# Optimization experiments

Hardware: AMD Instinct MI355X
Metric: run time of the kernel (lower is better)

## Reference

```python
import jax, jax.numpy as jnp
import numpy as np

EPS = 1e-5  # torch BatchNorm1d default eps


def setup_inputs() -> dict:
    key = jax.random.key(0)
    ks = jax.random.split(key, 8)
    B, H, D, DO = 8192, 8, 512, 256
    return {
        "x_concepts_encoded": jax.random.normal(ks[0], (B, H, D), dtype=jnp.float32),
        "relevance_weights": jax.random.uniform(ks[1], (B, H), dtype=jnp.float32),
        "bn_gamma": jax.random.uniform(ks[2], (D,), dtype=jnp.float32) + 0.5,
        "bn_beta": jax.random.normal(ks[3], (D,), dtype=jnp.float32) * 0.1,
        "bn_mean": jax.random.normal(ks[4], (D,), dtype=jnp.float32) * 0.1,
        "bn_var": jax.random.uniform(ks[5], (D,), dtype=jnp.float32) + 0.5,
        "W": jax.random.normal(ks[6], (DO, D), dtype=jnp.float32) / np.sqrt(D),
        "b": jax.random.normal(ks[7], (DO,), dtype=jnp.float32) * 0.01,
    }


def reference(x_concepts_encoded, relevance_weights, bn_gamma, bn_beta, bn_mean, bn_var, W, b):
    B, H = relevance_weights.shape
    x = x_concepts_encoded.reshape(B * H, -1)            # [B*H, D]
    # BatchNorm1d (inference: running stats) fused as scale/shift
    inv = bn_gamma * jax.lax.rsqrt(bn_var + EPS)
    h = x * inv + (bn_beta - bn_mean * inv)              # [B*H, D]
    # Swish
    h = h * jax.nn.sigmoid(h)
    # Linear
    out = h @ W.T + b                                    # [B*H, DO]
    # relevance-weighted sum over heads
    out = jnp.einsum('bhd,bh->bd', out.reshape(B, H, -1), relevance_weights)
    return out
```

## Files before the change

### kernel.cpp

```cpp
#include <hip/hip_runtime.h>
#include <hip/hip_bf16.h>

#define NB 8192
#define NH 8
#define ND 512
#define NO 256
#define ROWS 16

typedef __attribute__((ext_vector_type(8))) short short8;
typedef __attribute__((ext_vector_type(4))) float f32x4;

__device__ __align__(16) ushort g_wb[NO * ND];

__device__ __forceinline__ ushort f2bf(float f) {
    union { float f; unsigned u; } v; v.f = f;
    unsigned u = v.u;
    unsigned r = u + 0x7FFFu + ((u >> 16) & 1u);
    return (ushort)(r >> 16);
}

__global__ __launch_bounds__(256) void wcvt_kernel(const float* __restrict__ W) {
    int i = (blockIdx.x * 256 + threadIdx.x) * 4;
    float4 w = *(const float4*)(W + i);
    ushort4 o;
    o.x = f2bf(w.x); o.y = f2bf(w.y); o.z = f2bf(w.z); o.w = f2bf(w.w);
    *(ushort4*)(g_wb + i) = o;
}

__device__ __forceinline__ float swishf(float h) {
    return h * __builtin_amdgcn_rcpf(1.0f + __expf(-h));
}

__global__ __launch_bounds__(256) void fused_kernel(
    const float* __restrict__ x, const float* __restrict__ rw,
    const float* __restrict__ gamma, const float* __restrict__ beta,
    const float* __restrict__ mean, const float* __restrict__ var,
    const float* __restrict__ bias, float* __restrict__ out)
{
    __shared__ __align__(16) ushort yl[ROWS * ND];
    __shared__ float sumw[ROWS];

    const int tid = threadIdx.x;
    const int b0  = blockIdx.x * ROWS;

    const int d4 = tid & 127;
    const int rh = tid >> 7;
    const int d  = d4 * 4;

    float4 g4 = *(const float4*)(gamma + d);
    float4 v4 = *(const float4*)(var   + d);
    float4 be = *(const float4*)(beta  + d);
    float4 me = *(const float4*)(mean  + d);
    const float ix = g4.x * rsqrtf(v4.x + 1e-5f);
    const float iy = g4.y * rsqrtf(v4.y + 1e-5f);
    const float iz = g4.z * rsqrtf(v4.z + 1e-5f);
    const float iw = g4.w * rsqrtf(v4.w + 1e-5f);
    const float ox = be.x - me.x * ix;
    const float oy = be.y - me.y * iy;
    const float oz = be.z - me.z * iz;
    const float ow = be.w - me.w * iw;

    for (int rr = rh; rr < ROWS; rr += 2) {
        const int b = b0 + rr;
        const float* xr  = x + (size_t)b * (NH * ND) + d;
        const float* rwr = rw + b * NH;
        float ax = 0.f, ay = 0.f, az = 0.f, aw = 0.f, sumr = 0.f;
        #pragma unroll
        for (int h = 0; h < NH; ++h) {
            float4 xa = *(const float4*)(xr + h * ND);
            float wh = rwr[h];
            sumr += wh;
            ax += wh * swishf(xa.x * ix + ox);
            ay += wh * swishf(xa.y * iy + oy);
            az += wh * swishf(xa.z * iz + oz);
            aw += wh * swishf(xa.w * iw + ow);
        }
        const int addr = rr * 1024 + ((d * 2) ^ ((rr & 7) << 4));
        ushort4 o;
        o.x = f2bf(ax); o.y = f2bf(ay); o.z = f2bf(az); o.w = f2bf(aw);
        *(ushort4*)((char*)yl + addr) = o;
        if (d4 == 0) sumw[rr] = sumr;
    }
    __syncthreads();

    const int lane = tid & 63;
    const int wv   = tid >> 6;
    const int n0   = wv * 64;
    const int lr   = lane & 15;
    const int lk   = (lane >> 4) * 8;

    f32x4 acc0 = {0.f,0.f,0.f,0.f};
    f32x4 acc1 = {0.f,0.f,0.f,0.f};
    f32x4 acc2 = {0.f,0.f,0.f,0.f};
    f32x4 acc3 = {0.f,0.f,0.f,0.f};

    const char* ylb = (const char*)yl + lr * 1024;
    const int swz = (lr & 7) << 4;

    #pragma unroll 4
    for (int ks = 0; ks < 16; ++ks) {
        const int k0 = ks * 32;
        const int kb = (k0 + lk) * 2;
        short8 a = *(const short8*)(ylb + (kb ^ swz));
        const ushort* wp = g_wb + (size_t)(n0 + lr) * ND + k0 + lk;
        short8 bf0 = *(const short8*)(wp);
        short8 bf1 = *(const short8*)(wp + 16 * ND);
        short8 bf2 = *(const short8*)(wp + 32 * ND);
        short8 bf3 = *(const short8*)(wp + 48 * ND);
        acc0 = __builtin_amdgcn_mfma_f32_16x16x32_bf16(a, bf0, acc0, 0, 0, 0);
        acc1 = __builtin_amdgcn_mfma_f32_16x16x32_bf16(a, bf1, acc1, 0, 0, 0);
        acc2 = __builtin_amdgcn_mfma_f32_16x16x32_bf16(a, bf2, acc2, 0, 0, 0);
        acc3 = __builtin_amdgcn_mfma_f32_16x16x32_bf16(a, bf3, acc3, 0, 0, 0);
    }

    const int rbase = (lane >> 4) * 4;
    f32x4 accs[4] = {acc0, acc1, acc2, acc3};
    #pragma unroll
    for (int nf = 0; nf < 4; ++nf) {
        const int col = n0 + nf * 16 + lr;
        const float bn = bias[col];
        #pragma unroll
        for (int q = 0; q < 4; ++q) {
            const int r = rbase + q;
            out[(size_t)(b0 + r) * NO + col] = accs[nf][q] + bn * sumw[r];
        }
    }
}

extern "C" void kernel_launch(void* const* d_in, const int* in_sizes, int n_in,
                              void* d_out, int out_size, void* d_ws, size_t ws_size,
                              hipStream_t stream) {
    const float* x     = (const float*)d_in[0];
    const float* rw    = (const float*)d_in[1];
    const float* gamma = (const float*)d_in[2];
    const float* beta  = (const float*)d_in[3];
    const float* mean  = (const float*)d_in[4];
    const float* var   = (const float*)d_in[5];
    const float* W     = (const float*)d_in[6];
    const float* bias  = (const float*)d_in[7];
    float* out = (float*)d_out;

    hipLaunchKernelGGL(wcvt_kernel, dim3((NO * ND) / 1024), dim3(256), 0, stream, W);
    hipLaunchKernelGGL(fused_kernel, dim3(NB / ROWS), dim3(256), 0, stream,
                       x, rw, gamma, beta, mean, var, bias, out);
}
```

Baseline: 44.75 us.

## Double the block to 512 threads and software-prefetch the next row's inputs

Raises the block size to 512 threads, so four thread groups each handle four rows of the reduction stage. The loads of the next row's eight head vectors are issued before the current row is computed, to hide global-memory latency. Relevance weights are read as vectors and their sum is computed directly. In the GEMM stage each of the 8 waves now covers 32 output columns instead of 64, with a fully unrolled k loop. The risk is higher register pressure from holding two rows of prefetched float4 data under launch_bounds(512,4).

```diff
diff --git a/kernel.cpp b/kernel.cpp
--- a/kernel.cpp
+++ b/kernel.cpp
@@ -6,6 +6,7 @@
 #define ND 512
 #define NO 256
 #define ROWS 16
+#define TPB 512
 
 typedef __attribute__((ext_vector_type(8))) short short8;
 typedef __attribute__((ext_vector_type(4))) float f32x4;
@@ -31,7 +32,7 @@
     return h * __builtin_amdgcn_rcpf(1.0f + __expf(-h));
 }
 
-__global__ __launch_bounds__(256) void fused_kernel(
+__global__ __launch_bounds__(TPB, 4) void fused_kernel(
     const float* __restrict__ x, const float* __restrict__ rw,
     const float* __restrict__ gamma, const float* __restrict__ beta,
     const float* __restrict__ mean, const float* __restrict__ var,
@@ -60,44 +61,60 @@
     const float oz = be.z - me.z * iz;
     const float ow = be.w - me.w * iw;
 
-    for (int rr = rh; rr < ROWS; rr += 2) {
-        const int b = b0 + rr;
-        const float* xr  = x + (size_t)b * (NH * ND) + d;
-        const float* rwr = rw + b * NH;
-        float ax = 0.f, ay = 0.f, az = 0.f, aw = 0.f, sumr = 0.f;
+    const float* xr = x + (size_t)(b0 + rh) * (NH * ND) + d;
+    float4 cur[NH];
+    #pragma unroll
+    for (int h = 0; h < NH; ++h) cur[h] = *(const float4*)(xr + h * ND);
+
+    #pragma unroll
+    for (int it = 0; it < 4; ++it) {
+        const int rr = rh + it * 4;
+        float4 nxt[NH];
+        if (it < 3) {
+            const float* xn = xr + (size_t)4 * NH * ND;
+            #pragma unroll
+            for (int h = 0; h < NH; ++h) nxt[h] = *(const float4*)(xn + h * ND);
+        }
+        const float* rwr = rw + (b0 + rr) * NH;
+        float4 w0 = *(const float4*)(rwr);
+        float4 w1 = *(const float4*)(rwr + 4);
+        const float whv[NH] = {w0.x, w0.y, w0.z, w0.w, w1.x, w1.y, w1.z, w1.w};
+
+        float ax = 0.f, ay = 0.f, az = 0.f, aw = 0.f;
         #pragma unroll
         for (int h = 0; h < NH; ++h) {
-            float4 xa = *(const float4*)(xr + h * ND);
-            float wh = rwr[h];
-            sumr += wh;
-            ax += wh * swishf(xa.x * ix + ox);
-            ay += wh * swishf(xa.y * iy + oy);
-            az += wh * swishf(xa.z * iz + oz);
-            aw += wh * swishf(xa.w * iw + ow);
+            const float wh = whv[h];
+            ax += wh * swishf(cur[h].x * ix + ox);
+            ay += wh * swishf(cur[h].y * iy + oy);
+            az += wh * swishf(cur[h].z * iz + oz);
+            aw += wh * swishf(cur[h].w * iw + ow);
         }
         const int addr = rr * 1024 + ((d * 2) ^ ((rr & 7) << 4));
         ushort4 o;
         o.x = f2bf(ax); o.y = f2bf(ay); o.z = f2bf(az); o.w = f2bf(aw);
         *(ushort4*)((char*)yl + addr) = o;
-        if (d4 == 0) sumw[rr] = sumr;
+        if (d4 == 0)
+            sumw[rr] = w0.x + w0.y + w0.z + w0.w + w1.x + w1.y + w1.z + w1.w;
+
+        xr += (size_t)4 * NH * ND;
+        #pragma unroll
+        for (int h = 0; h < NH; ++h) cur[h] = nxt[h];
     }
     __syncthreads();
 
     const int lane = tid & 63;
     const int wv   = tid >> 6;
-    const int n0   = wv * 64;
+    const int n0   = wv * 32;
     const int lr   = lane & 15;
     const int lk   = (lane >> 4) * 8;
 
-    f32x4 acc0 = {0.f,0.f,0.f,0.f};
-    f32x4 acc1 = {0.f,0.f,0.f,0.f};
-    f32x4 acc2 = {0.f,0.f,0.f,0.f};
-    f32x4 acc3 = {0.f,0.f,0.f,0.f};
+    f32x4 acc0 = {0.f, 0.f, 0.f, 0.f};
+    f32x4 acc1 = {0.f, 0.f, 0.f, 0.f};
 
     const char* ylb = (const char*)yl + lr * 1024;
     const int swz = (lr & 7) << 4;
 
-    #pragma unroll 4
+    #pragma unroll
     for (int ks = 0; ks < 16; ++ks) {
         const int k0 = ks * 32;
         const int kb = (k0 + lk) * 2;
@@ -105,18 +122,14 @@
         const ushort* wp = g_wb + (size_t)(n0 + lr) * ND + k0 + lk;
         short8 bf0 = *(const short8*)(wp);
         short8 bf1 = *(const short8*)(wp + 16 * ND);
-        short8 bf2 = *(const short8*)(wp + 32 * ND);
-        short8 bf3 = *(const short8*)(wp + 48 * ND);
         acc0 = __builtin_amdgcn_mfma_f32_16x16x32_bf16(a, bf0, acc0, 0, 0, 0);
         acc1 = __builtin_amdgcn_mfma_f32_16x16x32_bf16(a, bf1, acc1, 0, 0, 0);
-        acc2 = __builtin_amdgcn_mfma_f32_16x16x32_bf16(a, bf2, acc2, 0, 0, 0);
-        acc3 = __builtin_amdgcn_mfma_f32_16x16x32_bf16(a, bf3, acc3, 0, 0, 0);
     }
 
     const int rbase = (lane >> 4) * 4;
-    f32x4 accs[4] = {acc0, acc1, acc2, acc3};
+    f32x4 accs[2] = {acc0, acc1};
     #pragma unroll
-    for (int nf = 0; nf < 4; ++nf) {
+    for (int nf = 0; nf < 2; ++nf) {
         const int col = n0 + nf * 16 + lr;
         const float bn = bias[col];
         #pragma unroll
@@ -141,6 +154,6 @@
     float* out = (float*)d_out;
 
     hipLaunchKernelGGL(wcvt_kernel, dim3((NO * ND) / 1024), dim3(256), 0, stream, W);
-    hipLaunchKernelGGL(fused_kernel, dim3(NB / ROWS), dim3(256), 0, stream,
+    hipLaunchKernelGGL(fused_kernel, dim3(NB / ROWS), dim3(512), 0, stream,
                        x, rw, gamma, beta, mean, var, bias, out);
 }
```

New measurement: 44.54 us. No clear change (-0.5%).
